# Kernel optimization log

Measured on AMD Instinct MI355X. Metric: run time of the kernel, lower is better.

The kernel has to match this reference:

```python
import jax, jax.numpy as jnp
import numpy as np

B, M, D = 16, 2048, 768
H = 12
Hd = D // H      # 64
HALF = Hd // 2   # 32
SCALE = Hd ** -0.5


def _rotate_half(x):
    # interleaved pair rotation: (x0,x1,x2,x3,...) -> (-x1,x0,-x3,x2,...)
    xe = x[..., ::2]
    xo = x[..., 1::2]
    return jnp.stack((-xo, xe), axis=-1).reshape(x.shape)


def _apply_rope2d(q, k, cos_y, sin_y, cos_x, sin_x):
    # q, k: [B, H, M, Hd]; caches: [M, HALF] -> broadcast as [1,1,M,HALF]
    cy = cos_y[None, None]
    sy = sin_y[None, None]
    cx = cos_x[None, None]
    sx = sin_x[None, None]
    qy, qx = q[..., :HALF], q[..., HALF:]
    ky, kx = k[..., :HALF], k[..., HALF:]
    qy = qy * cy + _rotate_half(qy) * sy
    qx = qx * cx + _rotate_half(qx) * sx
    ky = ky * cy + _rotate_half(ky) * sy
    kx = kx * cx + _rotate_half(kx) * sx
    return jnp.concatenate([qy, qx], axis=-1), jnp.concatenate([ky, kx], axis=-1)


def setup_inputs() -> dict:
    key = jax.random.key(0)
    ks = jax.random.split(key, 14)
    w_std = 0.02
    inp = {
        "x": jax.random.normal(ks[0], (B, M, D), dtype=jnp.float32),
        "cos_y": jax.random.uniform(ks[1], (M, HALF), dtype=jnp.float32),
        "sin_y": jax.random.uniform(ks[2], (M, HALF), dtype=jnp.float32),
        "cos_x": jax.random.uniform(ks[3], (M, HALF), dtype=jnp.float32),
        "sin_x": jax.random.uniform(ks[4], (M, HALF), dtype=jnp.float32),
        "Wq": jax.random.normal(ks[5], (D, D), dtype=jnp.float32) * w_std,
        "bq": jnp.zeros((D,), dtype=jnp.float32),
        "Wk": jax.random.normal(ks[6], (D, D), dtype=jnp.float32) * w_std,
        "bk": jnp.zeros((D,), dtype=jnp.float32),
        "Wv": jax.random.normal(ks[7], (D, D), dtype=jnp.float32) * w_std,
        "bv": jnp.zeros((D,), dtype=jnp.float32),
        "Wo": jax.random.normal(ks[8], (D, D), dtype=jnp.float32) * w_std,
        "bo": jnp.zeros((D,), dtype=jnp.float32),
    }
    return inp


def reference(x, cos_y, sin_y, cos_x, sin_x, Wq, bq, Wk, bk, Wv, bv, Wo, bo):
    # projections: [B, M, D] -> [B, H, M, Hd]
    def proj(W, b):
        return (x @ W + b).reshape(B, M, H, Hd).transpose(0, 2, 1, 3)

    q = proj(Wq, bq)
    k = proj(Wk, bk)
    v = proj(Wv, bv)
    q, k = _apply_rope2d(q, k, cos_y, sin_y, cos_x, sin_x)
    # scaled dot product attention (no mask, no dropout at inference)
    scores = jnp.einsum("bhqd,bhkd->bhqk", q, k) * SCALE
    attn = jax.nn.softmax(scores, axis=-1)
    out = jnp.einsum("bhqk,bhkd->bhqd", attn, v)
    out = out.transpose(0, 2, 1, 3).reshape(B, M, D)
    return out @ Wo + bo
```

## Files before the change

### kernel.cpp

```cpp
#include <hip/hip_runtime.h>
#include <hip/hip_bf16.h>
#include <stdint.h>

typedef __attribute__((ext_vector_type(4))) float f32x4;
typedef __attribute__((ext_vector_type(8))) short s16x8;
typedef __attribute__((ext_vector_type(4))) unsigned short u16x4;
typedef unsigned short u16;

#define NB 16
#define NM 2048
#define ND 768
#define NH 12
#define NROWS (NB*NM)
#define QSCALE 0.18033688011112042f

__device__ __forceinline__ u16 bf16rn(float v) {
  union { float f; uint32_t u; } x; x.f = v;
  uint32_t r = x.u + 0x7FFFu + ((x.u >> 16) & 1u);
  return (u16)(r >> 16);
}
__device__ __forceinline__ uint32_t f2u(float f) {
  union { float f; uint32_t u; } x; x.f = f; return x.u;
}

__device__ __forceinline__ f32x4 mfma16(s16x8 a, s16x8 b, f32x4 c) {
  return __builtin_amdgcn_mfma_f32_16x16x32_bf16(a, b, c, 0, 0, 0);
}

#define GLOAD16(g, s) __builtin_amdgcn_global_load_lds( \
    (__attribute__((address_space(1))) void*)(g), \
    (__attribute__((address_space(3))) void*)(s), 16, 0, 0)

__global__ void k_splitx_hi(const float* __restrict__ x, u16* __restrict__ xh) {
  const int n4 = NROWS * ND / 4;
  for (int i = blockIdx.x * blockDim.x + threadIdx.x; i < n4;
       i += gridDim.x * blockDim.x) {
    f32x4 v = ((const f32x4*)x)[i];
    u16x4 hv;
#pragma unroll
    for (int j = 0; j < 4; ++j) hv[j] = bf16rn(v[j]);
    ((u16x4*)xh)[i] = hv;
  }
}

__global__ void k_prep_w(const float* __restrict__ Wq, const float* __restrict__ Wk,
                         const float* __restrict__ Wv, const float* __restrict__ Wo,
                         u16* __restrict__ wth) {
  int idx = blockIdx.x * 256 + threadIdx.x;
  if (idx >= 3072 * 768) return;
  int j = idx / 768, k = idx % 768;
  int mat = j / 768;
  int jj = j - mat * 768;
  const float* W = (mat == 0) ? Wq : (mat == 1) ? Wk : (mat == 2) ? Wv : Wo;
  wth[idx] = bf16rn(W[k * 768 + jj]);
}

__global__ __launch_bounds__(256, 3) void k_qkv(
    const u16* __restrict__ xh, const u16* __restrict__ wth,
    const float* __restrict__ bq, const float* __restrict__ bk,
    const float* __restrict__ bv,
    const float* __restrict__ cy, const float* __restrict__ sy,
    const float* __restrict__ cx, const float* __restrict__ sx,
    u16* __restrict__ Qh, u16* __restrict__ Kh, u16* __restrict__ Vth)
{
  __shared__ char lds[32768];
  const int t = threadIdx.x, l = t & 63, w = t >> 6;
  const int lr = l & 15, lg = l >> 4;
  const int bid = blockIdx.x;
  const int swz = (bid & 7) * 576 + (bid >> 3);
  const int n0 = (swz / 18) * 128;
  const int j0 = (swz % 18) * 128;
  const int wr = w >> 1, wc = w & 1;
  f32x4 acc[4][4] = {};

  for (int kt = 0; kt < 12; ++kt) {
    const int k0 = kt * 64;
    __syncthreads();
#pragma unroll
    for (int i = 0; i < 4; ++i) {
      int o = (i * 4 + w) * 1024 + l * 16;
      int r = o >> 7;
      int gb = (o & 127) ^ ((r & 7) << 4);
      size_t ga = ((size_t)(n0 + r) * 768 + k0) * 2 + gb;
      size_t gw = ((size_t)(j0 + r) * 768 + k0) * 2 + gb;
      GLOAD16((const char*)xh + ga, lds + o);
      GLOAD16((const char*)wth + gw, lds + 16384 + o);
    }
    __syncthreads();
#pragma unroll
    for (int s = 0; s < 2; ++s) {
      s16x8 ah[4], bh_[4];
#pragma unroll
      for (int mi = 0; mi < 4; ++mi) {
        int r = wr * 64 + mi * 16 + lr;
        int off = r * 128 + ((s * 64 + lg * 16) ^ ((r & 7) << 4));
        ah[mi] = *(const s16x8*)(lds + off);
      }
#pragma unroll
      for (int ni = 0; ni < 4; ++ni) {
        int r = wc * 64 + ni * 16 + lr;
        int off = r * 128 + ((s * 64 + lg * 16) ^ ((r & 7) << 4));
        bh_[ni] = *(const s16x8*)(lds + 16384 + off);
      }
#pragma unroll
      for (int mi = 0; mi < 4; ++mi)
#pragma unroll
        for (int ni = 0; ni < 4; ++ni)
          acc[mi][ni] = mfma16(ah[mi], bh_[ni], acc[mi][ni]);
    }
  }

#pragma unroll
  for (int ni = 0; ni < 4; ++ni) {
    const int col = j0 + wc * 64 + ni * 16 + lr;
    const int mat = col / 768;
    const int cj = col % 768;
    const int h = cj >> 6, d = cj & 63;
    const float bias = (mat == 0 ? bq : mat == 1 ? bk : bv)[cj];
    const float* ct = (d < 32) ? cy : cx;
    const float* st = (d < 32) ? sy : sx;
    const int e = d & 31;
    const bool odd = (d & 1) != 0;
#pragma unroll
    for (int mi = 0; mi < 4; ++mi) {
      const int nbase = n0 + wr * 64 + mi * 16 + lg * 4;
      if (mat == 2) {
        const int b = nbase >> 11, m = nbase & 2047;
        const size_t off = ((size_t)(b * 12 + h) * 64 + d) * 2048 + m;
        u16x4 hv;
#pragma unroll
        for (int r = 0; r < 4; ++r) hv[r] = bf16rn(acc[mi][ni][r] + bias);
        *(u16x4*)(Vth + off) = hv;
      } else {
#pragma unroll
        for (int r = 0; r < 4; ++r) {
          const int n = nbase + r;
          const int b = n >> 11, m = n & 2047;
          float v = acc[mi][ni][r] + bias;
          float p = __shfl_xor(v, 1);
          float c = ct[m * 32 + e], sn = st[m * 32 + e];
          float ov = odd ? (v * c + p * sn) : (v * c - p * sn);
          if (mat == 0) ov *= QSCALE;
          const size_t off = ((size_t)(b * 12 + h) * 2048 + m) * 64 + d;
          (mat == 0 ? Qh : Kh)[off] = bf16rn(ov);
        }
      }
    }
  }
}

__global__ __launch_bounds__(256, 4) void k_attn(
    const u16* __restrict__ Qh, const u16* __restrict__ Kh,
    const u16* __restrict__ Vth, u16* __restrict__ Oh)
{
  __shared__ char lds[32768];
  const int t = threadIdx.x, l = t & 63, w = t >> 6;
  const int lr = l & 15, lg = l >> 4;
  const int bid = blockIdx.x;
  const int swz = (bid & 7) * 384 + (bid >> 3);
  const int bh = swz >> 4;
  const int q0 = (swz & 15) * 128;
  const size_t base = (size_t)bh * (2048 * 64);

  s16x8 qf[2][2];
#pragma unroll
  for (int mi = 0; mi < 2; ++mi)
#pragma unroll
    for (int ks = 0; ks < 2; ++ks) {
      size_t off = base + (size_t)(q0 + w * 32 + mi * 16 + lr) * 64 + ks * 32 + lg * 8;
      qf[mi][ks] = *(const s16x8*)(Qh + off);
    }

  f32x4 oacc[2][4] = {};
  float lsum[2] = {0.f, 0.f};
  const f32x4 fz = {0.f, 0.f, 0.f, 0.f};

  auto STAGE = [&](int b, int kc) {
    const int km0 = kc * 64;
#pragma unroll
    for (int i = 0; i < 2; ++i) {
      int o = (i * 4 + w) * 1024 + l * 16;
      int r = o >> 7;
      int gb = (o & 127) ^ ((r & 7) << 4);
      size_t gk = (base + (size_t)(km0 + r) * 64) * 2 + gb;
      size_t gv = (base + (size_t)r * 2048 + km0) * 2 + gb;
      GLOAD16((const char*)Kh + gk, lds + b * 16384 + o);
      GLOAD16((const char*)Vth + gv, lds + b * 16384 + 8192 + o);
    }
  };

  STAGE(0, 0);
  asm volatile("s_waitcnt vmcnt(0)" ::: "memory");
  __syncthreads();

  for (int kc = 0; kc < 32; ++kc) {
    const int cur = kc & 1;
    if (kc < 31) STAGE(cur ^ 1, kc + 1);
    const char* kv = lds + cur * 16384;

    f32x4 s[4][2];
    {
      s16x8 kb[4];
#pragma unroll
      for (int ni = 0; ni < 4; ++ni) {
        int r = ni * 16 + lr;
        kb[ni] = *(const s16x8*)(kv + r * 128 + ((lg * 16) ^ ((r & 7) << 4)));
      }
#pragma unroll
      for (int ni = 0; ni < 4; ++ni)
#pragma unroll
        for (int mi = 0; mi < 2; ++mi)
          s[ni][mi] = mfma16(kb[ni], qf[mi][0], fz);
#pragma unroll
      for (int ni = 0; ni < 4; ++ni) {
        int r = ni * 16 + lr;
        kb[ni] = *(const s16x8*)(kv + r * 128 + ((64 + lg * 16) ^ ((r & 7) << 4)));
      }
#pragma unroll
      for (int ni = 0; ni < 4; ++ni)
#pragma unroll
        for (int mi = 0; mi < 2; ++mi)
          s[ni][mi] = mfma16(kb[ni], qf[mi][1], s[ni][mi]);
    }

    s16x8 paf[2][2];
#pragma unroll
    for (int mi = 0; mi < 2; ++mi) {
      uint32_t pk[4][2];
      float rs = 0.f;
#pragma unroll
      for (int ni = 0; ni < 4; ++ni) {
        float p0 = __builtin_amdgcn_exp2f(s[ni][mi][0]);
        float p1 = __builtin_amdgcn_exp2f(s[ni][mi][1]);
        float p2 = __builtin_amdgcn_exp2f(s[ni][mi][2]);
        float p3 = __builtin_amdgcn_exp2f(s[ni][mi][3]);
        rs += (p0 + p1) + (p2 + p3);
        asm("v_cvt_pk_bf16_f32 %0, %1, %2" : "=v"(pk[ni][0]) : "v"(p0), "v"(p1));
        asm("v_cvt_pk_bf16_f32 %0, %1, %2" : "=v"(pk[ni][1]) : "v"(p2), "v"(p3));
      }
      lsum[mi] += rs;
#pragma unroll
      for (int c = 0; c < 2; ++c) {
        uint32_t x0 = pk[2 * c][0], y0 = pk[2 * c + 1][0];
        uint32_t x1 = pk[2 * c][1], y1 = pk[2 * c + 1][1];
        asm("v_permlane32_swap_b32 %0, %1" : "+v"(x0), "+v"(y0));
        asm("v_permlane32_swap_b32 %0, %1" : "+v"(x1), "+v"(y1));
        asm("v_permlane16_swap_b32 %0, %1" : "+v"(x0), "+v"(y0));
        asm("v_permlane16_swap_b32 %0, %1" : "+v"(x1), "+v"(y1));
        union { uint32_t u[4]; s16x8 v; } fr;
        fr.u[0] = x0; fr.u[1] = x1; fr.u[2] = y0; fr.u[3] = y1;
        paf[mi][c] = fr.v;
      }
    }

#pragma unroll
    for (int c = 0; c < 2; ++c) {
      s16x8 vf[4];
#pragma unroll
      for (int di = 0; di < 4; ++di) {
        int r = di * 16 + lr;
        int off = r * 128 + ((c * 64 + lg * 16) ^ ((r & 7) << 4));
        vf[di] = *(const s16x8*)(kv + 8192 + off);
      }
#pragma unroll
      for (int mi = 0; mi < 2; ++mi)
#pragma unroll
        for (int di = 0; di < 4; ++di)
          oacc[mi][di] = mfma16(paf[mi][c], vf[di], oacc[mi][di]);
    }

    asm volatile("s_waitcnt vmcnt(0)" ::: "memory");
    __syncthreads();
  }

  float ls[2];
#pragma unroll
  for (int mi = 0; mi < 2; ++mi) {
    float v = lsum[mi];
    v += __shfl_xor(v, 16);
    v += __shfl_xor(v, 32);
    ls[mi] = v;
  }

  const int bb = bh / 12, hh = bh % 12;
#pragma unroll
  for (int mi = 0; mi < 2; ++mi)
#pragma unroll
    for (int i = 0; i < 4; ++i) {
      float tot = __shfl(ls[mi], lg * 4 + i);
      float inv = __builtin_amdgcn_rcpf(tot);
      size_t nrow = (size_t)bb * 2048 + q0 + w * 32 + mi * 16 + lg * 4 + i;
#pragma unroll
      for (int di = 0; di < 4; ++di) {
        float v = oacc[mi][di][i] * inv;
        size_t off = nrow * 768 + hh * 64 + di * 16 + lr;
        Oh[off] = bf16rn(v);
      }
    }
}

__global__ __launch_bounds__(256, 3) void k_out(
    const u16* __restrict__ oh, const u16* __restrict__ wth,
    const float* __restrict__ bo, float* __restrict__ out)
{
  __shared__ char lds[32768];
  const int t = threadIdx.x, l = t & 63, w = t >> 6;
  const int lr = l & 15, lg = l >> 4;
  const int bid = blockIdx.x;
  const int swz = (bid & 7) * 192 + (bid >> 3);
  const int n0 = (swz / 6) * 128;
  const int j0 = (swz % 6) * 128;
  const int wr = w >> 1, wc = w & 1;
  f32x4 acc[4][4] = {};

  for (int kt = 0; kt < 12; ++kt) {
    const int k0 = kt * 64;
    __syncthreads();
#pragma unroll
    for (int i = 0; i < 4; ++i) {
      int o = (i * 4 + w) * 1024 + l * 16;
      int r = o >> 7;
      int gb = (o & 127) ^ ((r & 7) << 4);
      size_t ga = ((size_t)(n0 + r) * 768 + k0) * 2 + gb;
      size_t gw = ((size_t)(2304 + j0 + r) * 768 + k0) * 2 + gb;
      GLOAD16((const char*)oh + ga, lds + o);
      GLOAD16((const char*)wth + gw, lds + 16384 + o);
    }
    __syncthreads();
#pragma unroll
    for (int s = 0; s < 2; ++s) {
      s16x8 ah[4], bh_[4];
#pragma unroll
      for (int mi = 0; mi < 4; ++mi) {
        int r = wr * 64 + mi * 16 + lr;
        int off = r * 128 + ((s * 64 + lg * 16) ^ ((r & 7) << 4));
        ah[mi] = *(const s16x8*)(lds + off);
      }
#pragma unroll
      for (int ni = 0; ni < 4; ++ni) {
        int r = wc * 64 + ni * 16 + lr;
        int off = r * 128 + ((s * 64 + lg * 16) ^ ((r & 7) << 4));
        bh_[ni] = *(const s16x8*)(lds + 16384 + off);
      }
#pragma unroll
      for (int mi = 0; mi < 4; ++mi)
#pragma unroll
        for (int ni = 0; ni < 4; ++ni)
          acc[mi][ni] = mfma16(ah[mi], bh_[ni], acc[mi][ni]);
    }
  }
#pragma unroll
  for (int ni = 0; ni < 4; ++ni) {
    const int col = j0 + wc * 64 + ni * 16 + lr;
    const float bias = bo[col];
#pragma unroll
    for (int mi = 0; mi < 4; ++mi) {
      const int nb = n0 + wr * 64 + mi * 16 + lg * 4;
#pragma unroll
      for (int r = 0; r < 4; ++r)
        out[(size_t)(nb + r) * 768 + col] = acc[mi][ni][r] + bias;
    }
  }
}

extern "C" void kernel_launch(void* const* d_in, const int* in_sizes, int n_in,
                              void* d_out, int out_size, void* d_ws, size_t ws_size,
                              hipStream_t stream) {
  const float* x  = (const float*)d_in[0];
  const float* cy = (const float*)d_in[1];
  const float* sy = (const float*)d_in[2];
  const float* cx = (const float*)d_in[3];
  const float* sx = (const float*)d_in[4];
  const float* Wq = (const float*)d_in[5];
  const float* bq = (const float*)d_in[6];
  const float* Wk = (const float*)d_in[7];
  const float* bk = (const float*)d_in[8];
  const float* Wv = (const float*)d_in[9];
  const float* bv = (const float*)d_in[10];
  const float* Wo = (const float*)d_in[11];
  const float* bo = (const float*)d_in[12];
  float* out = (float*)d_out;

  char* ws = (char*)d_ws;
  size_t o = 0;
  const size_t SZ_X = (size_t)NROWS * ND * 2;
  const size_t SZ_W = (size_t)3072 * 768 * 2;
  u16* Xh  = (u16*)(ws + o); o += SZ_X;
  u16* Wth = (u16*)(ws + o); o += SZ_W;
  u16* Vth = (u16*)(ws + o); o += SZ_X;
  u16* Oh  = Xh;

  u16* Qh = (u16*)d_out;
  u16* Kh = Qh + (size_t)NROWS * 768;

  k_splitx_hi<<<2048, 256, 0, stream>>>(x, Xh);
  k_prep_w<<<(3072 * 768 + 255) / 256, 256, 0, stream>>>(Wq, Wk, Wv, Wo, Wth);
  k_qkv<<<4608, 256, 0, stream>>>(Xh, Wth, bq, bk, bv,
                                  cy, sy, cx, sx, Qh, Kh, Vth);
  k_attn<<<3072, 256, 0, stream>>>(Qh, Kh, Vth, Oh);
  k_out<<<1536, 256, 0, stream>>>(Oh, Wth, bo, out);
}
```

Baseline: 457.0 us.

## Compute softmax row sums via MFMA with ones vector and precompute staging addresses

```diff
diff --git a/kernel.cpp b/kernel.cpp
--- a/kernel.cpp
+++ b/kernel.cpp
@@ -18,9 +18,6 @@
   union { float f; uint32_t u; } x; x.f = v;
   uint32_t r = x.u + 0x7FFFu + ((x.u >> 16) & 1u);
   return (u16)(r >> 16);
-}
-__device__ __forceinline__ uint32_t f2u(float f) {
-  union { float f; uint32_t u; } x; x.f = f; return x.u;
 }
 
 __device__ __forceinline__ f32x4 mfma16(s16x8 a, s16x8 b, f32x4 c) {
@@ -172,30 +169,43 @@
     }
 
   f32x4 oacc[2][4] = {};
-  float lsum[2] = {0.f, 0.f};
+  f32x4 sacc[2] = {};
   const f32x4 fz = {0.f, 0.f, 0.f, 0.f};
-
-  auto STAGE = [&](int b, int kc) {
-    const int km0 = kc * 64;
-#pragma unroll
-    for (int i = 0; i < 2; ++i) {
-      int o = (i * 4 + w) * 1024 + l * 16;
-      int r = o >> 7;
-      int gb = (o & 127) ^ ((r & 7) << 4);
-      size_t gk = (base + (size_t)(km0 + r) * 64) * 2 + gb;
-      size_t gv = (base + (size_t)r * 2048 + km0) * 2 + gb;
-      GLOAD16((const char*)Kh + gk, lds + b * 16384 + o);
-      GLOAD16((const char*)Vth + gv, lds + b * 16384 + 8192 + o);
-    }
+  s16x8 ones;
+#pragma unroll
+  for (int j = 0; j < 8; ++j) ones[j] = (short)0x3F80;
+
+  int lo0, lo1;
+  const char *ka0, *ka1, *va0, *va1;
+  {
+    int o0 = w * 1024 + l * 16;
+    int o1 = o0 + 4096;
+    int r0 = o0 >> 7, r1 = o1 >> 7;
+    int gb0 = (o0 & 127) ^ ((r0 & 7) << 4);
+    int gb1 = (o1 & 127) ^ ((r1 & 7) << 4);
+    lo0 = o0; lo1 = o1;
+    ka0 = (const char*)Kh + (base + (size_t)r0 * 64) * 2 + gb0;
+    ka1 = (const char*)Kh + (base + (size_t)r1 * 64) * 2 + gb1;
+    va0 = (const char*)Vth + (base + (size_t)r0 * 2048) * 2 + gb0;
+    va1 = (const char*)Vth + (base + (size_t)r1 * 2048) * 2 + gb1;
+  }
+  auto STAGE = [&](int b) {
+    char* dst = lds + b * 16384;
+    GLOAD16(ka0, dst + lo0);
+    GLOAD16(ka1, dst + lo1);
+    GLOAD16(va0, dst + 8192 + lo0);
+    GLOAD16(va1, dst + 8192 + lo1);
+    ka0 += 8192; ka1 += 8192;
+    va0 += 128;  va1 += 128;
   };
 
-  STAGE(0, 0);
+  STAGE(0);
   asm volatile("s_waitcnt vmcnt(0)" ::: "memory");
   __syncthreads();
 
   for (int kc = 0; kc < 32; ++kc) {
     const int cur = kc & 1;
-    if (kc < 31) STAGE(cur ^ 1, kc + 1);
+    if (kc < 31) STAGE(cur ^ 1);
     const char* kv = lds + cur * 16384;
 
     f32x4 s[4][2];
@@ -227,18 +237,15 @@
 #pragma unroll
     for (int mi = 0; mi < 2; ++mi) {
       uint32_t pk[4][2];
-      float rs = 0.f;
 #pragma unroll
       for (int ni = 0; ni < 4; ++ni) {
         float p0 = __builtin_amdgcn_exp2f(s[ni][mi][0]);
         float p1 = __builtin_amdgcn_exp2f(s[ni][mi][1]);
         float p2 = __builtin_amdgcn_exp2f(s[ni][mi][2]);
         float p3 = __builtin_amdgcn_exp2f(s[ni][mi][3]);
-        rs += (p0 + p1) + (p2 + p3);
         asm("v_cvt_pk_bf16_f32 %0, %1, %2" : "=v"(pk[ni][0]) : "v"(p0), "v"(p1));
         asm("v_cvt_pk_bf16_f32 %0, %1, %2" : "=v"(pk[ni][1]) : "v"(p2), "v"(p3));
       }
-      lsum[mi] += rs;
 #pragma unroll
       for (int c = 0; c < 2; ++c) {
         uint32_t x0 = pk[2 * c][0], y0 = pk[2 * c + 1][0];
@@ -263,32 +270,24 @@
         vf[di] = *(const s16x8*)(kv + 8192 + off);
       }
 #pragma unroll
-      for (int mi = 0; mi < 2; ++mi)
+      for (int mi = 0; mi < 2; ++mi) {
+        sacc[mi] = mfma16(paf[mi][c], ones, sacc[mi]);
 #pragma unroll
         for (int di = 0; di < 4; ++di)
           oacc[mi][di] = mfma16(paf[mi][c], vf[di], oacc[mi][di]);
+      }
     }
 
     asm volatile("s_waitcnt vmcnt(0)" ::: "memory");
     __syncthreads();
   }
 
-  float ls[2];
-#pragma unroll
-  for (int mi = 0; mi < 2; ++mi) {
-    float v = lsum[mi];
-    v += __shfl_xor(v, 16);
-    v += __shfl_xor(v, 32);
-    ls[mi] = v;
-  }
-
   const int bb = bh / 12, hh = bh % 12;
 #pragma unroll
   for (int mi = 0; mi < 2; ++mi)
 #pragma unroll
     for (int i = 0; i < 4; ++i) {
-      float tot = __shfl(ls[mi], lg * 4 + i);
-      float inv = __builtin_amdgcn_rcpf(tot);
+      float inv = __builtin_amdgcn_rcpf(sacc[mi][i]);
       size_t nrow = (size_t)bb * 2048 + q0 + w * 32 + mi * 16 + lg * 4 + i;
 #pragma unroll
       for (int di = 0; di < 4; ++di) {
```

Measured after the change: 440.9 us. 3.5% less time.
